# Kernel optimization log

Measured on AMD Instinct MI355X. Metric: run time of the kernel, lower is better.

Reference implementation:

```python
import jax, jax.numpy as jnp
import numpy as np
import math

B, T, C = 4, 2048, 1024
N_HEAD = 16


def setup_inputs() -> dict:
    key = jax.random.key(0)
    k1, k2, k3 = jax.random.split(key, 3)
    x = jax.random.normal(k1, (B, T, C), dtype=jnp.float32)
    W_attn = jax.random.normal(k2, (C, 3 * C), dtype=jnp.float32) * (1.0 / math.sqrt(C))
    b_attn = jnp.zeros((3 * C,), dtype=jnp.float32)
    W_proj = jax.random.normal(k3, (C, C), dtype=jnp.float32) * (1.0 / math.sqrt(C))
    b_proj = jnp.zeros((C,), dtype=jnp.float32)
    return {"x": x, "W_attn": W_attn, "b_attn": b_attn, "W_proj": W_proj, "b_proj": b_proj}


def reference(x, W_attn, b_attn, W_proj, b_proj):
    b, t, c = x.shape
    hs = c // N_HEAD  # head size
    qkv = x @ W_attn + b_attn  # [B,T,3C]
    q, k, v = jnp.split(qkv, 3, axis=-1)
    # [B,T,C] -> [B,H,T,hs]
    q = q.reshape(b, t, N_HEAD, hs).transpose(0, 2, 1, 3)
    k = k.reshape(b, t, N_HEAD, hs).transpose(0, 2, 1, 3)
    v = v.reshape(b, t, N_HEAD, hs).transpose(0, 2, 1, 3)
    att = jnp.einsum('bhqd,bhkd->bhqk', q, k) / math.sqrt(hs)  # [B,H,T,T]
    causal = jnp.tril(jnp.ones((t, t), dtype=bool))
    att = jnp.where(causal[None, None, :, :], att, -jnp.inf)
    att = jax.nn.softmax(att, axis=-1)
    y = jnp.einsum('bhqk,bhkd->bhqd', att, v)  # [B,H,T,hs]
    y = y.transpose(0, 2, 1, 3).reshape(b, t, c)
    return y @ W_proj + b_proj
```

## Files before the change

kernel.cpp:

```cpp
#include <hip/hip_runtime.h>


typedef __bf16 bf16_t;
typedef __bf16 bf16x8 __attribute__((ext_vector_type(8)));
typedef __bf16 bf16x4 __attribute__((ext_vector_type(4)));
typedef float  f32x4  __attribute__((ext_vector_type(4)));

#define MFMA16(a, b, c) __builtin_amdgcn_mfma_f32_16x16x32_bf16((a), (b), (c), 0, 0, 0)

static __device__ __forceinline__ void gld_lds16(const bf16_t* g, void* l) {
  __builtin_amdgcn_global_load_lds(
      (const __attribute__((address_space(1))) void*)(const void*)g,
      (__attribute__((address_space(3))) void*)l, 16, 0, 0);
}

static __device__ __forceinline__ bf16x8 ldv8(const void* p) {
  return *reinterpret_cast<const bf16x8*>(p);
}

static __device__ __forceinline__ float exp2_hw(float x) {
  float r;
  asm("v_exp_f32 %0, %1" : "=v"(r) : "v"(x));
  return r;
}

__global__ __launch_bounds__(256) void cvt_f32_bf16(const float* __restrict__ in,
                                                    bf16_t* __restrict__ out, int n4) {
  int i = blockIdx.x * 256 + threadIdx.x;
  if (i < n4) {
    float4 v = reinterpret_cast<const float4*>(in)[i];
    bf16x4 o;
    o[0] = (bf16_t)v.x; o[1] = (bf16_t)v.y; o[2] = (bf16_t)v.z; o[3] = (bf16_t)v.w;
    reinterpret_cast<bf16x4*>(out)[i] = o;
  }
}

__global__ __launch_bounds__(256) void transpose_cvt(const float* __restrict__ in,
                                                     bf16_t* __restrict__ out,
                                                     int Kd, int Nd) {
  __shared__ float tile[32][33];
  int tx = threadIdx.x, ty = threadIdx.y;
  int n0 = blockIdx.x * 32, k0 = blockIdx.y * 32;
#pragma unroll
  for (int i = 0; i < 4; ++i)
    tile[ty + i * 8][tx] = in[(size_t)(k0 + ty + i * 8) * Nd + (n0 + tx)];
  __syncthreads();
#pragma unroll
  for (int i = 0; i < 4; ++i)
    out[(size_t)(n0 + ty + i * 8) * Kd + (k0 + tx)] = (bf16_t)tile[tx][ty + i * 8];
}

template <int MODE>
__global__ __launch_bounds__(256) void gemm_bf16(
    const bf16_t* __restrict__ A, const bf16_t* __restrict__ Bt,
    const float* __restrict__ bias, int M, int N, int K,
    bf16_t* __restrict__ Qo, bf16_t* __restrict__ Ko, bf16_t* __restrict__ Vt,
    float* __restrict__ Co) {
  __shared__ alignas(16) char lds[32768];

  const int tid = threadIdx.x;
  const int wave = tid >> 6, lane = tid & 63;
  const int wm = wave >> 1, wn = wave & 1;
  const int l16 = lane & 15, kb = lane >> 4;

  const int nbx = gridDim.x;
  const int lb = blockIdx.y * nbx + blockIdx.x;
  const int c = lb & 7;
  const int ii = lb >> 3;
  const int rPer = gridDim.y >> 3;
  const int tmt = c * rPer + (ii % rPer);
  const int tnt = ii / rPer;
  const int tm0 = tmt * 128, tn0 = tnt * 128;

  const int srow = wave * 8 + (lane >> 3);
  const int sp = lane & 7;

  f32x4 acc[4][4] = {};

  for (int k0 = 0; k0 < K; k0 += 64) {
    __syncthreads();
#pragma unroll
    for (int inst = 0; inst < 4; ++inst) {
      const int row = inst * 32 + srow;
      const int chunk = (sp ^ (row & 7)) * 8;
      gld_lds16(A + (size_t)(tm0 + row) * K + k0 + chunk,
                &lds[inst * 4096 + wave * 1024]);
      gld_lds16(Bt + (size_t)(tn0 + row) * K + k0 + chunk,
                &lds[16384 + inst * 4096 + wave * 1024]);
    }
    __syncthreads();
#pragma unroll
    for (int kc = 0; kc < 2; ++kc) {
      bf16x8 af[4], bfr[4];
#pragma unroll
      for (int mi = 0; mi < 4; ++mi) {
        const int row = wm * 64 + mi * 16 + l16;
        const int slot = (kc * 4 + kb) ^ (row & 7);
        af[mi] = ldv8(&lds[row * 128 + slot * 16]);
      }
#pragma unroll
      for (int ni = 0; ni < 4; ++ni) {
        const int row = wn * 64 + ni * 16 + l16;
        const int slot = (kc * 4 + kb) ^ (row & 7);
        bfr[ni] = ldv8(&lds[16384 + row * 128 + slot * 16]);
      }
#pragma unroll
      for (int mi = 0; mi < 4; ++mi)
#pragma unroll
        for (int ni = 0; ni < 4; ++ni)
          acc[mi][ni] = MFMA16(af[mi], bfr[ni], acc[mi][ni]);
    }
  }

#pragma unroll
  for (int ni = 0; ni < 4; ++ni) {
    const int n = tn0 + wn * 64 + ni * 16 + l16;
    const float bv = bias[n];
#pragma unroll
    for (int mi = 0; mi < 4; ++mi) {
#pragma unroll
      for (int j = 0; j < 4; ++j) {
        const int m = tm0 + wm * 64 + mi * 16 + kb * 4 + j;
        const float v = acc[mi][ni][j] + bv;
        if constexpr (MODE == 0) {
          const int which = n >> 10, hn = n & 1023;
          const int h = hn >> 6, d = hn & 63;
          const int b = m >> 11, t = m & 2047;
          const size_t bh = (size_t)(b * 16 + h);
          if (which == 0)
            Qo[(bh * 2048 + t) * 64 + d] = (bf16_t)(v * 0.18033688011112042f);
          else if (which == 1)
            Ko[(bh * 2048 + t) * 64 + d] = (bf16_t)v;
          else
            Vt[(bh * 64 + d) * 2048 + t] = (bf16_t)v;
        } else {
          Co[(size_t)m * N + n] = v;
        }
      }
    }
  }
}

__global__ __launch_bounds__(256) void attn_fwd(const bf16_t* __restrict__ Qg,
                                                const bf16_t* __restrict__ Kg,
                                                const bf16_t* __restrict__ Vtg,
                                                bf16_t* __restrict__ Yg) {
  __shared__ alignas(16) char lds[24576];

  const int tid = threadIdx.x;
  const int wave = tid >> 6, lane = tid & 63;
  const int l16 = lane & 15, kb = lane >> 4;
  const int l8 = l16 & 7;
  const float NEG_INF = -__builtin_inff();

  const int n = blockIdx.x;
  const int bh = (n & 7) * 8 + ((n >> 3) & 7);
  const int qt = 31 - (n >> 6);
  const size_t base = (size_t)bh * (2048 * 64);
  const int b = bh >> 4, h = bh & 15;

  const int srow = tid >> 3;
  const int schunk = (tid & 7) ^ (srow & 7);
  const bf16_t* Ksrc = Kg + base + (size_t)srow * 64 + schunk * 8;
  const bf16_t* Vsrc = Vtg + base + (size_t)srow * 2048 + schunk * 8;

  auto stageK = [&](int buf, int kv0) {
    char* kd = lds + buf * 8192 + wave * 1024;
    const bf16_t* ks = Ksrc + (size_t)kv0 * 64;
    gld_lds16(ks, kd);
    gld_lds16(ks + 2048, kd + 4096);
  };
  auto stageV = [&](int kv0) {
    char* vd = lds + 16384 + wave * 1024;
    const bf16_t* vs = Vsrc + kv0;
    gld_lds16(vs, vd);
    gld_lds16(vs + 65536, vd + 4096);
  };

  const int q0 = qt * 64 + wave * 16;
  const int q = q0 + l16;
  const int trips = qt + 1;

  const bf16x8 qf0 = ldv8(Qg + base + (size_t)q * 64 + kb * 8);
  const bf16x8 qf1 = ldv8(Qg + base + (size_t)q * 64 + 32 + kb * 8);

  f32x4 o[4] = {};
  float m_r = NEG_INF, l_r = 0.f;

  stageK(0, 0);
  stageV(0);
  asm volatile("s_waitcnt vmcnt(0)" ::: "memory");
  __builtin_amdgcn_s_barrier();
  __builtin_amdgcn_sched_barrier(0);

  int cur = 0;
  for (int t = 0; t < trips; ++t) {
    const int kv0 = t * 64;
    const bool more = (t + 1 < trips);
    if (more) stageK(cur ^ 1, kv0 + 64);

    const char* Kb = lds + cur * 8192;
    const char* Vb = lds + 16384;

    bf16x8 kf[8];
#pragma unroll
    for (int i = 0; i < 4; ++i) {
      const int row = i * 16 + l16;
#pragma unroll
      for (int kc = 0; kc < 2; ++kc)
        kf[i * 2 + kc] = ldv8(Kb + row * 128 + (((kc * 4 + kb) ^ (row & 7)) * 16));
    }

    f32x4 s[4] = {};
    __builtin_amdgcn_s_setprio(1);
#pragma unroll
    for (int i = 0; i < 4; ++i) {
      s[i] = MFMA16(kf[i * 2 + 0], qf0, s[i]);
      s[i] = MFMA16(kf[i * 2 + 1], qf1, s[i]);
    }
    __builtin_amdgcn_s_setprio(0);

    bf16x8 vf[8];
#pragma unroll
    for (int i = 0; i < 4; ++i) {
      const int row = i * 16 + l16;
#pragma unroll
      for (int kc = 0; kc < 2; ++kc)
        vf[i * 2 + kc] = ldv8(Vb + row * 128 + (((kc * 4 + kb) ^ (row & 7)) * 16));
    }

    float pm[4];
    if (t == qt) {
#pragma unroll
      for (int i = 0; i < 4; ++i) {
        f32x4 sv = s[i];
#pragma unroll
        for (int j = 0; j < 4; ++j)
          if (kv0 + i * 16 + kb * 4 + j > q) sv[j] = NEG_INF;
        s[i] = sv;
        pm[i] = fmaxf(fmaxf(sv[0], sv[1]), fmaxf(sv[2], sv[3]));
      }
    } else {
#pragma unroll
      for (int i = 0; i < 4; ++i)
        pm[i] = fmaxf(fmaxf(s[i][0], s[i][1]), fmaxf(s[i][2], s[i][3]));
    }
    float mx = fmaxf(fmaxf(pm[0], pm[1]), fmaxf(pm[2], pm[3]));
    if (__any(mx > m_r + 8.0f)) {
      mx = fmaxf(mx, __shfl_xor(mx, 16));
      mx = fmaxf(mx, __shfl_xor(mx, 32));
      const float mn = fmaxf(m_r, mx);
      const float sc = exp2_hw(m_r - mn);
      l_r *= sc;
#pragma unroll
      for (int i = 0; i < 4; ++i) {
        o[i][0] *= sc; o[i][1] *= sc; o[i][2] *= sc; o[i][3] *= sc;
      }
      m_r = mn;
    }
    float ss = 0.f;
    bf16x4 pw[4];
#pragma unroll
    for (int i = 0; i < 4; ++i)
#pragma unroll
      for (int j = 0; j < 4; ++j) {
        const float p = exp2_hw(s[i][j] - m_r);
        ss += p;
        pw[i][j] = (bf16_t)p;
      }
    l_r += ss;

    asm volatile("s_waitcnt lgkmcnt(0)" ::: "memory");
    __builtin_amdgcn_s_barrier();
    __builtin_amdgcn_sched_barrier(0);
    if (more) stageV(kv0 + 64);

    char* Pw = lds + cur * 8192 + wave * 2048;
#pragma unroll
    for (int i = 0; i < 4; ++i) {
      const int phys = (i * 2 + (kb >> 1)) ^ l8;
      *reinterpret_cast<bf16x4*>(Pw + l16 * 128 + phys * 16 + (kb & 1) * 8) = pw[i];
    }
    const bf16x8 pb0 = ldv8(Pw + l16 * 128 + ((kb ^ l8) * 16));
    const bf16x8 pb1 = ldv8(Pw + l16 * 128 + (((4 + kb) ^ l8) * 16));

    __builtin_amdgcn_s_setprio(1);
#pragma unroll
    for (int i = 0; i < 4; ++i) {
      o[i] = MFMA16(vf[i * 2 + 0], pb0, o[i]);
      o[i] = MFMA16(vf[i * 2 + 1], pb1, o[i]);
    }
    __builtin_amdgcn_s_setprio(0);

    asm volatile("s_waitcnt vmcnt(0)" ::: "memory");
    __builtin_amdgcn_s_barrier();
    __builtin_amdgcn_sched_barrier(0);
    cur ^= 1;
  }

  float lt = l_r + __shfl_xor(l_r, 16);
  lt += __shfl_xor(lt, 32);
  const float inv = 1.0f / lt;
  bf16_t* yrow = Yg + ((size_t)(b * 2048 + q)) * 1024 + h * 64;
#pragma unroll
  for (int i = 0; i < 4; ++i) {
    bf16x4 yv;
    yv[0] = (bf16_t)(o[i][0] * inv);
    yv[1] = (bf16_t)(o[i][1] * inv);
    yv[2] = (bf16_t)(o[i][2] * inv);
    yv[3] = (bf16_t)(o[i][3] * inv);
    *reinterpret_cast<bf16x4*>(yrow + i * 16 + kb * 4) = yv;
  }
}

extern "C" void kernel_launch(void* const* d_in, const int* in_sizes, int n_in,
                              void* d_out, int out_size, void* d_ws, size_t ws_size,
                              hipStream_t stream) {
  const float* x = (const float*)d_in[0];
  const float* W_attn = (const float*)d_in[1];
  const float* b_attn = (const float*)d_in[2];
  const float* W_proj = (const float*)d_in[3];
  const float* b_proj = (const float*)d_in[4];
  float* out = (float*)d_out;

  char* ws = (char*)d_ws;
  bf16_t* xb  = (bf16_t*)(ws + 0);
  bf16_t* WaT = (bf16_t*)(ws + 16777216);
  bf16_t* WpT = (bf16_t*)(ws + 23068672);
  bf16_t* Qb  = (bf16_t*)(ws + 25165824);
  bf16_t* Kb  = (bf16_t*)(ws + 41943040);
  bf16_t* Vt  = (bf16_t*)(ws + 58720256);
  bf16_t* Yb  = (bf16_t*)(ws + 75497472);

  cvt_f32_bf16<<<8192, 256, 0, stream>>>(x, xb, 8192 * 1024 / 4);
  transpose_cvt<<<dim3(96, 32), dim3(32, 8), 0, stream>>>(W_attn, WaT, 1024, 3072);
  transpose_cvt<<<dim3(32, 32), dim3(32, 8), 0, stream>>>(W_proj, WpT, 1024, 1024);

  gemm_bf16<0><<<dim3(24, 64), 256, 0, stream>>>(xb, WaT, b_attn, 8192, 3072, 1024,
                                                 Qb, Kb, Vt, nullptr);

  attn_fwd<<<2048, 256, 0, stream>>>(Qb, Kb, Vt, Yb);

  gemm_bf16<1><<<dim3(8, 64), 256, 0, stream>>>(Yb, WpT, b_proj, 8192, 1024, 1024,
                                                nullptr, nullptr, nullptr, out);
}
```

Before: 183.9 us.

## Use 256x256-tile, 8-wave pipelined GEMM for QKV projection

Replaces the shared 128x128 GEMM template with a dedicated QKV kernel that uses 256x256 tiles, 512 threads, 128KB of double-buffered LDS, and a quarter-phase schedule. Each phase interleaves async global-to-LDS staging of the next K tile with MFMA work, and raises wave priority around the MFMAs. The aim is more data reuse per tile and better overlap of loads with math. It risks lower occupancy and too few blocks (384) to fill the machine, plus register pressure from 32 accumulators per thread. The output projection keeps the old kernel, now specialised without the mode template.

```diff
diff --git a/kernel.cpp b/kernel.cpp
--- a/kernel.cpp
+++ b/kernel.cpp
@@ -50,11 +50,129 @@
     out[(size_t)(n0 + ty + i * 8) * Kd + (k0 + tx)] = (bf16_t)tile[tx][ty + i * 8];
 }
 
-template <int MODE>
-__global__ __launch_bounds__(256) void gemm_bf16(
+__global__ __launch_bounds__(512) void gemm_qkv(
     const bf16_t* __restrict__ A, const bf16_t* __restrict__ Bt,
     const float* __restrict__ bias, int M, int N, int K,
-    bf16_t* __restrict__ Qo, bf16_t* __restrict__ Ko, bf16_t* __restrict__ Vt,
+    bf16_t* __restrict__ Qo, bf16_t* __restrict__ Ko, bf16_t* __restrict__ Vt) {
+  __shared__ alignas(16) char lds[131072];
+
+  const int tid = threadIdx.x;
+  const int wave = tid >> 6, lane = tid & 63;
+  const int wm = wave >> 2, wn = wave & 3;
+  const int l16 = lane & 15, kb = lane >> 4;
+  const int r7 = l16 & 7;
+
+  const int nbx = gridDim.x;
+  const int lb = blockIdx.y * nbx + blockIdx.x;
+  const int c = lb & 7;
+  const int ii = lb >> 3;
+  const int rPer = gridDim.y >> 3;
+  const int tmt = c * rPer + (ii % rPer);
+  const int tnt = ii / rPer;
+  const int tm0 = tmt * 256, tn0 = tnt * 256;
+
+  const int srow = tid >> 3;
+  const int sch = (tid & 7) ^ (srow & 7);
+  const bf16_t* aR = A + (size_t)(tm0 + srow) * K + sch * 8;
+  const bf16_t* bR = Bt + (size_t)(tn0 + srow) * K + sch * 8;
+
+  auto stageAh = [&](int buf, int h, int kt) {
+    char* d = lds + buf * 65536 + h * 16384 + wave * 1024;
+    const bf16_t* s = aR + (size_t)(h * 128) * K + kt * 64;
+    gld_lds16(s, d);
+    gld_lds16(s + (size_t)64 * K, d + 8192);
+  };
+  auto stageBh = [&](int buf, int h, int kt) {
+    char* d = lds + buf * 65536 + 32768 + h * 16384 + wave * 1024;
+    const bf16_t* s = bR + (size_t)(h * 128) * K + kt * 64;
+    gld_lds16(s, d);
+    gld_lds16(s + (size_t)64 * K, d + 8192);
+  };
+
+  f32x4 acc[8][4] = {};
+  const int NK = K >> 6;
+
+  stageAh(0, 0, 0); stageAh(0, 1, 0); stageBh(0, 0, 0); stageBh(0, 1, 0);
+  asm volatile("s_waitcnt vmcnt(0)" ::: "memory");
+  __builtin_amdgcn_s_barrier();
+  __builtin_amdgcn_sched_barrier(0);
+
+  for (int kt = 0; kt < NK; ++kt) {
+    const int buf = kt & 1;
+    const bool more = (kt + 1 < NK);
+    const char* Abase = lds + buf * 65536 + wm * 16384;
+    const char* Bbase = lds + buf * 65536 + 32768 + (wn >> 1) * 16384 + (wn & 1) * 8192;
+
+#define QPHASE(QM, QN, STAGE_STMT, TAIL_STMT)                                   \
+    {                                                                           \
+      bf16x8 af[4][2], bfr[2][2];                                               \
+      _Pragma("unroll")                                                         \
+      for (int mi = 0; mi < 4; ++mi)                                            \
+        _Pragma("unroll")                                                       \
+        for (int kc = 0; kc < 2; ++kc)                                          \
+          af[mi][kc] = ldv8(Abase + (QM) * 8192 + (mi * 16 + l16) * 128 +       \
+                            (((kc * 4 + kb) ^ r7) * 16));                       \
+      _Pragma("unroll")                                                         \
+      for (int ni = 0; ni < 2; ++ni)                                            \
+        _Pragma("unroll")                                                       \
+        for (int kc = 0; kc < 2; ++kc)                                          \
+          bfr[ni][kc] = ldv8(Bbase + ((QN) * 32 + ni * 16 + l16) * 128 +        \
+                             (((kc * 4 + kb) ^ r7) * 16));                      \
+      STAGE_STMT;                                                               \
+      __builtin_amdgcn_s_barrier();                                             \
+      asm volatile("s_waitcnt lgkmcnt(0)" ::: "memory");                        \
+      __builtin_amdgcn_sched_barrier(0);                                        \
+      __builtin_amdgcn_s_setprio(1);                                            \
+      _Pragma("unroll")                                                         \
+      for (int mi = 0; mi < 4; ++mi)                                            \
+        _Pragma("unroll")                                                       \
+        for (int ni = 0; ni < 2; ++ni)                                          \
+          _Pragma("unroll")                                                     \
+          for (int kc = 0; kc < 2; ++kc)                                        \
+            acc[(QM) * 4 + mi][(QN) * 2 + ni] =                                 \
+                MFMA16(af[mi][kc], bfr[ni][kc], acc[(QM) * 4 + mi][(QN) * 2 + ni]); \
+      __builtin_amdgcn_s_setprio(0);                                            \
+      TAIL_STMT;                                                                \
+      __builtin_amdgcn_s_barrier();                                             \
+      __builtin_amdgcn_sched_barrier(0);                                        \
+    }
+
+    QPHASE(0, 0, if (more) stageAh(buf ^ 1, 0, kt + 1), )
+    QPHASE(0, 1, if (more) stageAh(buf ^ 1, 1, kt + 1), )
+    QPHASE(1, 0, if (more) stageBh(buf ^ 1, 0, kt + 1), )
+    QPHASE(1, 1, if (more) stageBh(buf ^ 1, 1, kt + 1),
+           if (more) asm volatile("s_waitcnt vmcnt(0)" ::: "memory"))
+#undef QPHASE
+  }
+
+#pragma unroll
+  for (int ni = 0; ni < 4; ++ni) {
+    const int n = tn0 + wn * 64 + ni * 16 + l16;
+    const float bv = bias[n];
+#pragma unroll
+    for (int mi = 0; mi < 8; ++mi) {
+#pragma unroll
+      for (int j = 0; j < 4; ++j) {
+        const int m = tm0 + wm * 128 + mi * 16 + kb * 4 + j;
+        const float v = acc[mi][ni][j] + bv;
+        const int which = n >> 10, hn = n & 1023;
+        const int h = hn >> 6, d = hn & 63;
+        const int b = m >> 11, t = m & 2047;
+        const size_t bh = (size_t)(b * 16 + h);
+        if (which == 0)
+          Qo[(bh * 2048 + t) * 64 + d] = (bf16_t)(v * 0.18033688011112042f);
+        else if (which == 1)
+          Ko[(bh * 2048 + t) * 64 + d] = (bf16_t)v;
+        else
+          Vt[(bh * 64 + d) * 2048 + t] = (bf16_t)v;
+      }
+    }
+  }
+}
+
+__global__ __launch_bounds__(256) void gemm_proj(
+    const bf16_t* __restrict__ A, const bf16_t* __restrict__ Bt,
+    const float* __restrict__ bias, int M, int N, int K,
     float* __restrict__ Co) {
   __shared__ alignas(16) char lds[32768];
 
@@ -121,21 +239,7 @@
 #pragma unroll
       for (int j = 0; j < 4; ++j) {
         const int m = tm0 + wm * 64 + mi * 16 + kb * 4 + j;
-        const float v = acc[mi][ni][j] + bv;
-        if constexpr (MODE == 0) {
-          const int which = n >> 10, hn = n & 1023;
-          const int h = hn >> 6, d = hn & 63;
-          const int b = m >> 11, t = m & 2047;
-          const size_t bh = (size_t)(b * 16 + h);
-          if (which == 0)
-            Qo[(bh * 2048 + t) * 64 + d] = (bf16_t)(v * 0.18033688011112042f);
-          else if (which == 1)
-            Ko[(bh * 2048 + t) * 64 + d] = (bf16_t)v;
-          else
-            Vt[(bh * 64 + d) * 2048 + t] = (bf16_t)v;
-        } else {
-          Co[(size_t)m * N + n] = v;
-        }
+        Co[(size_t)m * N + n] = acc[mi][ni][j] + bv;
       }
     }
   }
@@ -336,11 +440,10 @@
   transpose_cvt<<<dim3(96, 32), dim3(32, 8), 0, stream>>>(W_attn, WaT, 1024, 3072);
   transpose_cvt<<<dim3(32, 32), dim3(32, 8), 0, stream>>>(W_proj, WpT, 1024, 1024);
 
-  gemm_bf16<0><<<dim3(24, 64), 256, 0, stream>>>(xb, WaT, b_attn, 8192, 3072, 1024,
-                                                 Qb, Kb, Vt, nullptr);
+  gemm_qkv<<<dim3(12, 32), 512, 0, stream>>>(xb, WaT, b_attn, 8192, 3072, 1024,
+                                             Qb, Kb, Vt);
 
   attn_fwd<<<2048, 256, 0, stream>>>(Qb, Kb, Vt, Yb);
 
-  gemm_bf16<1><<<dim3(8, 64), 256, 0, stream>>>(Yb, WpT, b_proj, 8192, 1024, 1024,
-                                                nullptr, nullptr, nullptr, out);
-}
+  gemm_proj<<<dim3(8, 64), 256, 0, stream>>>(Yb, WpT, b_proj, 8192, 1024, 1024, out);
+}
```

Result: slower. 213.2 us (+16.0%).
